# Kernel tuning notes

Hardware: AMD Instinct MI355X
Metric: run time of the kernel (lower is better)

Reference implementation:

```python
import jax, jax.numpy as jnp
import numpy as np

B, C, H, W = 2, 512, 30, 40
K = 64
PATCH, STRIDE = 4, 1
EPS = 1e-12  # torch F.normalize eps


def _l2norm(v, axis):
    n = jnp.sqrt(jnp.sum(v * v, axis=axis, keepdims=True))
    return v / jnp.maximum(n, EPS)


def setup_inputs() -> dict:
    key = jax.random.key(0)
    k1, k2, k3 = jax.random.split(key, 3)
    x = jax.random.normal(k1, (B, C, H, W), dtype=jnp.float32)
    conv_w = jax.random.normal(k2, (K, C), dtype=jnp.float32) * 0.05  # 1x1 conv weight, no bias (vlad_v2=False)
    centroids = jax.random.normal(k3, (K, C), dtype=jnp.float32)
    return {"x": x, "conv_w": conv_w, "centroids": centroids}


def reference(x, conv_w, centroids):
    b, c, h, w = x.shape
    k = centroids.shape[0]
    # input L2 normalization along channels
    xn = _l2norm(x, axis=1)
    # soft assignment: 1x1 conv + softmax over clusters
    soft = jax.nn.softmax(jnp.einsum('kc,bchw->bkhw', conv_w, xn), axis=1)
    # weighted residuals [B,K,C,H,W] (fused; original loops over K)
    resid = (xn[:, None, :, :, :] - centroids[None, :, :, None, None]) * soft[:, :, None, :, :]
    # global VLAD: sum over spatial
    vlad_global = jnp.sum(resid, axis=(-2, -1))  # [B,K,C]
    vlad_global = _l2norm(vlad_global, axis=2).reshape(b, -1)
    vlad_global = _l2norm(vlad_global, axis=1)
    # integral image over [B, K*C, H, W]
    r = resid.reshape(b, k * c, h, w)
    integ = jnp.cumsum(jnp.cumsum(r, axis=-1), axis=-2)
    integ = jnp.pad(integ, ((0, 0), (0, 0), (1, 0), (1, 0)))  # [B,KC,H+1,W+1]
    # box-sum via integral-image differences (equiv. to the dilated 2x2 grouped conv)
    p, s = PATCH, STRIDE
    hp = (h - p) // s + 1
    wp = (w - p) // s + 1
    ye, xe = (hp - 1) * s + 1, (wp - 1) * s + 1
    tl = integ[:, :, 0:ye:s, 0:xe:s]
    tr = integ[:, :, 0:ye:s, p:p + xe:s]
    bl = integ[:, :, p:p + ye:s, 0:xe:s]
    br = integ[:, :, p:p + ye:s, p:p + xe:s]
    box = (br - tr - bl + tl) / (p * p)  # [B,KC,hp,wp]
    v = box.reshape(b, k, c, hp * wp)
    v = _l2norm(v, axis=2)  # intra-cluster norm
    v = v.reshape(b, k * c, hp * wp)
    vlad_local = _l2norm(v, axis=1)  # [B, K*C, hp*wp]
    return (vlad_local, vlad_global)
```

## Files before the change

kernel.cpp:

```cpp
#include <hip/hip_runtime.h>
#include <math.h>

#define BB 2
#define CC 512
#define HH 30
#define WW 40
#define KK 64
#define NPIX (HH*WW)
#define HP 27
#define WP 37
#define NP (HP*WP)
#define LEPS 1e-12f

#define PADW 168
#define SROW 680
#define NCG 8

__global__ __launch_bounds__(512) void k_norm_soft(
    const float* __restrict__ x, const float* __restrict__ convw,
    float* __restrict__ xn, float* __restrict__ soft)
{
  const int h = blockIdx.x, b = blockIdx.y;
  const int t = threadIdx.x;
  __shared__ float xc[64][41];
  __shared__ float cw[64][65];
  __shared__ float Lb[KK][WW + 1];
  __shared__ float psum[12][WW];
  __shared__ float invn[WW];
  __shared__ float mx[WW], Zs[WW];

  const size_t xbase = (size_t)b * CC * NPIX + (size_t)h * WW;

  if (t < 480) {
    const int w = t % 40, part = t / 40;
    float s = 0.f;
    for (int c = part; c < CC; c += 12) {
      const float v = x[xbase + (size_t)c * NPIX + w];
      s = fmaf(v, v, s);
    }
    psum[part][w] = s;
  }
  __syncthreads();
  if (t < 40) {
    float s = 0.f;
    #pragma unroll
    for (int p = 0; p < 12; ++p) s += psum[p][t];
    invn[t] = 1.f / fmaxf(sqrtf(s), LEPS);
  }
  __syncthreads();

  const int k = t & 63, wp = t >> 6;
  float acc[5] = {0.f, 0.f, 0.f, 0.f, 0.f};
  for (int cb = 0; cb < CC; cb += 64) {
    #pragma unroll
    for (int n = 0; n < 5; ++n) {
      const int idx = t + 512 * n;
      const int c = idx / 40, w = idx % 40;
      const float v = x[xbase + (size_t)(cb + c) * NPIX + w] * invn[w];
      xc[c][w] = v;
      xn[xbase + (size_t)(cb + c) * NPIX + w] = v;
    }
    #pragma unroll
    for (int n = 0; n < 8; ++n) {
      const int idx = t + 512 * n;
      const int kk2 = idx >> 6, c2 = idx & 63;
      cw[kk2][c2] = convw[(size_t)kk2 * CC + cb + c2];
    }
    __syncthreads();
    #pragma unroll 1
    for (int c = 0; c < 64; ++c) {
      const float cv = cw[k][c];
      #pragma unroll
      for (int n = 0; n < 5; ++n)
        acc[n] = fmaf(cv, xc[c][wp + 8 * n], acc[n]);
    }
    __syncthreads();
  }
  #pragma unroll
  for (int n = 0; n < 5; ++n) Lb[k][wp + 8 * n] = acc[n];
  __syncthreads();
  if (t < 40) {
    float m = -1e30f;
    for (int kk2 = 0; kk2 < KK; ++kk2) m = fmaxf(m, Lb[kk2][t]);
    float Z = 0.f;
    for (int kk2 = 0; kk2 < KK; ++kk2) Z += expf(Lb[kk2][t] - m);
    mx[t] = m; Zs[t] = Z;
  }
  __syncthreads();
  const size_t sbase = (size_t)b * KK * NPIX + (size_t)h * WW;
  #pragma unroll
  for (int n = 0; n < 5; ++n) {
    const int idx = t + 512 * n;
    const int kk2 = idx / 40, w = idx % 40;
    soft[sbase + (size_t)kk2 * NPIX + w] = expf(Lb[kk2][w] - mx[w]) / Zs[w];
  }
}

__global__ __launch_bounds__(256) void k_global(
    const float* __restrict__ xn, const float* __restrict__ soft,
    const float* __restrict__ cent, float* __restrict__ ghat)
{
  const int k = blockIdx.x, b = blockIdx.y, t = threadIdx.x;
  __shared__ float sb[NPIX];
  __shared__ float red[256];
  const float* srow = soft + ((size_t)b * KK + k) * NPIX;
  for (int i2 = t; i2 < NPIX; i2 += 256) sb[i2] = srow[i2];
  __syncthreads();
  float p = 0.f;
  for (int i2 = t; i2 < NPIX; i2 += 256) p += sb[i2];
  red[t] = p;
  __syncthreads();
  for (int s = 128; s > 0; s >>= 1) { if (t < s) red[t] += red[t + s]; __syncthreads(); }
  const float Sg = red[0];
  __syncthreads();

  const int c0 = t, c1 = t + 256;
  const float* x0 = xn + ((size_t)b * CC + c0) * NPIX;
  const float* x1 = xn + ((size_t)b * CC + c1) * NPIX;
  float a0 = 0.f, a1 = 0.f;
  for (int p4 = 0; p4 < NPIX; p4 += 4) {
    const float4 s4 = *(const float4*)&sb[p4];
    const float4 v0 = *(const float4*)(x0 + p4);
    const float4 v1 = *(const float4*)(x1 + p4);
    a0 = fmaf(s4.x, v0.x, a0); a0 = fmaf(s4.y, v0.y, a0);
    a0 = fmaf(s4.z, v0.z, a0); a0 = fmaf(s4.w, v0.w, a0);
    a1 = fmaf(s4.x, v1.x, a1); a1 = fmaf(s4.y, v1.y, a1);
    a1 = fmaf(s4.z, v1.z, a1); a1 = fmaf(s4.w, v1.w, a1);
  }
  const float g0 = a0 - cent[(size_t)k * CC + c0] * Sg;
  const float g1 = a1 - cent[(size_t)k * CC + c1] * Sg;
  red[t] = g0 * g0 + g1 * g1;
  __syncthreads();
  for (int s = 128; s > 0; s >>= 1) { if (t < s) red[t] += red[t + s]; __syncthreads(); }
  const float inv = 1.f / fmaxf(sqrtf(red[0]), LEPS);
  float* gr = ghat + ((size_t)b * KK + k) * CC;
  gr[c0] = g0 * inv; gr[c1] = g1 * inv;
}

__global__ __launch_bounds__(256) void k_global2(
    const float* __restrict__ ghat, float* __restrict__ outg)
{
  const int b = blockIdx.x, t = threadIdx.x;
  __shared__ float red[256];
  const float* gb = ghat + (size_t)b * KK * CC;
  float p = 0.f;
  for (int i2 = t; i2 < KK * CC; i2 += 256) { const float v = gb[i2]; p = fmaf(v, v, p); }
  red[t] = p;
  __syncthreads();
  for (int s = 128; s > 0; s >>= 1) { if (t < s) red[t] += red[t + s]; __syncthreads(); }
  const float inv = 1.f / fmaxf(sqrtf(red[0]), LEPS);
  for (int i2 = t; i2 < KK * CC; i2 += 256)
    outg[(size_t)b * KK * CC + i2] = gb[i2] * inv;
}

template<int PHASE>
__global__ __launch_bounds__(320, 2) void k_local2(
    const float* __restrict__ xn, const float* __restrict__ soft,
    const float* __restrict__ cent, float* __restrict__ sp,
    const float* __restrict__ fs, float* __restrict__ out)
{
  const int cg = blockIdx.x;
  const int k0 = blockIdx.y * 4;
  const int bz = blockIdx.z;
  const int b = bz >> 1, iz = bz & 1;
  const int i0 = iz * 14;
  const int n_i = iz ? 13 : 14;
  const int c0 = cg * 64;
  const int t = threadIdx.x;
  const int c8 = t / 40, j = t % 40;

  __shared__ float xn_l[64][PADW];
  __shared__ float soft_l[4][SROW];
  __shared__ float cent_l[4][64];
  __shared__ float red[PHASE == 0 ? 8*4*40 : 4];

  {
    const int len = (NPIX - i0 * 40) < SROW ? (NPIX - i0 * 40) : SROW;
    const int nf4 = len >> 2;
    for (int u = t; u < 4 * nf4; u += 320) {
      const int kk = u / nf4, q = u - kk * nf4;
      *(float4*)&soft_l[kk][q * 4] =
        *(const float4*)&soft[((size_t)(b * KK + k0 + kk)) * NPIX + i0 * 40 + q * 4];
    }
  }
  if (t < 256) cent_l[t >> 6][t & 63] = cent[(size_t)(k0 + (t >> 6)) * CC + c0 + (t & 63)];

  const int sc = t / 10, sq = t % 10;
  #pragma unroll
  for (int rr = 0; rr < 4; ++rr) {
    const int row = i0 + rr;
    const int slot = (row & 3) * 40 + sq * 4;
    *(float4*)&xn_l[sc][slot] =
      *(const float4*)&xn[((size_t)(b * CC + c0 + sc)) * NPIX + (size_t)row * 40 + sq * 4];
    *(float4*)&xn_l[sc + 32][slot] =
      *(const float4*)&xn[((size_t)(b * CC + c0 + sc + 32)) * NPIX + (size_t)row * 40 + sq * 4];
  }
  __syncthreads();

  for (int ii = 0; ii < n_i; ++ii) {
    const int i = i0 + ii;

    const int nrow = (i + 4 < HH) ? (i + 4) : (HH - 1);
    const float4 st0 = *(const float4*)&xn[((size_t)(b * CC + c0 + sc)) * NPIX
                                           + (size_t)nrow * 40 + sq * 4];
    const float4 st1 = *(const float4*)&xn[((size_t)(b * CC + c0 + sc + 32)) * NPIX
                                           + (size_t)nrow * 40 + sq * 4];
    float fsv[4];
    if (PHASE == 1) {
      #pragma unroll
      for (int kk = 0; kk < 4; ++kk)
        fsv[kk] = (j < WP)
          ? fs[((size_t)(b * KK + k0 + kk)) * NP + (size_t)i * WP + j] : 0.f;
    }

    float sloc[4] = {0.f, 0.f, 0.f, 0.f};
    if (j < WP) {
      float acc[8][4];
      float Ssum[4] = {0.f, 0.f, 0.f, 0.f};
      #pragma unroll
      for (int cc = 0; cc < 8; ++cc)
        #pragma unroll
        for (int kk = 0; kk < 4; ++kk) acc[cc][kk] = 0.f;
      #pragma unroll
      for (int r = 0; r < 4; ++r) {
        const int xo = ((i + r) & 3) * 40 + j;
        const int so = (ii + r) * 40 + j;
        float sv[4][4];
        #pragma unroll
        for (int kk = 0; kk < 4; ++kk) {
          #pragma unroll
          for (int dx = 0; dx < 4; ++dx) sv[kk][dx] = soft_l[kk][so + dx];
          Ssum[kk] += (sv[kk][0] + sv[kk][1]) + (sv[kk][2] + sv[kk][3]);
        }
        #pragma unroll
        for (int cc = 0; cc < 8; ++cc) {
          const float x0 = xn_l[c8 * 8 + cc][xo + 0];
          const float x1 = xn_l[c8 * 8 + cc][xo + 1];
          const float x2 = xn_l[c8 * 8 + cc][xo + 2];
          const float x3 = xn_l[c8 * 8 + cc][xo + 3];
          #pragma unroll
          for (int kk = 0; kk < 4; ++kk) {
            float a = acc[cc][kk];
            a = fmaf(x0, sv[kk][0], a);
            a = fmaf(x1, sv[kk][1], a);
            a = fmaf(x2, sv[kk][2], a);
            a = fmaf(x3, sv[kk][3], a);
            acc[cc][kk] = a;
          }
        }
      }
      #pragma unroll
      for (int kk = 0; kk < 4; ++kk) {
        const float Sv = Ssum[kk];
        #pragma unroll
        for (int cc = 0; cc < 8; ++cc) {
          const float raw = fmaf(-cent_l[kk][c8 * 8 + cc], Sv, acc[cc][kk]);
          if (PHASE == 0)
            sloc[kk] = fmaf(raw, raw, sloc[kk]);
          else
            out[((size_t)((b * KK + k0 + kk) * CC + c0 + c8 * 8 + cc)) * NP
                + (size_t)i * WP + j] = raw * fsv[kk];
        }
      }
    }
    if (PHASE == 0) {
      #pragma unroll
      for (int kk = 0; kk < 4; ++kk) red[(c8 * 4 + kk) * 40 + j] = sloc[kk];
    }
    __syncthreads();

    {
      const int slot = ((i + 4) & 3) * 40 + sq * 4;
      *(float4*)&xn_l[sc][slot] = st0;
      *(float4*)&xn_l[sc + 32][slot] = st1;
    }
    if (PHASE == 0 && t < 160) {
      const int kk = t / 40, jj = t % 40;
      if (jj < WP) {
        float s = 0.f;
        #pragma unroll
        for (int g = 0; g < 8; ++g) s += red[(g * 4 + kk) * 40 + jj];
        sp[(((size_t)(b * KK + k0 + kk)) * NCG + cg) * NP + (size_t)i * WP + jj] = s;
      }
    }
    __syncthreads();
  }
}

__global__ __launch_bounds__(256) void k_nf_a(
    const float* __restrict__ sp, float* __restrict__ ssq)
{
  const int u = blockIdx.x * 256 + threadIdx.x;
  if (u >= BB * KK * NP) return;
  const int bk = u / NP, p = u - bk * NP;
  float s = 0.f;
  #pragma unroll
  for (int g = 0; g < NCG; ++g)
    s += sp[((size_t)bk * NCG + g) * NP + p];
  ssq[u] = s;
}

__global__ __launch_bounds__(256) void k_nf_b(
    const float* __restrict__ ssq, float* __restrict__ fs)
{
  const int b = blockIdx.y, t = threadIdx.x;
  const int k = t >> 2, dp = t & 3;
  const int p = blockIdx.x * 4 + dp;
  __shared__ float red[64][4];
  __shared__ float inv2s[4];
  const bool ok = p < NP;
  const float sr = ok ? ssq[((size_t)(b * KK + k)) * NP + p] : 0.f;
  const float iv = 1.f / fmaxf(sqrtf(sr) * 0.0625f, LEPS);
  red[k][dp] = sr * (1.f / 256.f) * iv * iv;
  __syncthreads();
  if (t < 4) {
    float s = 0.f;
    #pragma unroll
    for (int kk = 0; kk < 64; ++kk) s += red[kk][t];
    inv2s[t] = 1.f / fmaxf(sqrtf(s), LEPS);
  }
  __syncthreads();
  if (ok)
    fs[((size_t)(b * KK + k)) * NP + p] = 0.0625f * iv * inv2s[dp];
}

extern "C" void kernel_launch(void* const* d_in, const int* in_sizes, int n_in,
                              void* d_out, int out_size, void* d_ws, size_t ws_size,
                              hipStream_t stream)
{
  const float* x     = (const float*)d_in[0];
  const float* convw = (const float*)d_in[1];
  const float* cent  = (const float*)d_in[2];
  float* out = (float*)d_out;
  float* ws  = (float*)d_ws;

  float* xn   = ws;
  float* soft = xn   + (size_t)BB * CC * NPIX;
  float* fs   = soft + (size_t)BB * KK * NPIX;
  float* ghat = fs   + (size_t)BB * KK * NP;
  float* ssq  = ghat + (size_t)BB * KK * CC;
  float* sp   = ssq  + (size_t)BB * KK * NP;

  k_norm_soft<<<dim3(HH, BB), 512, 0, stream>>>(x, convw, xn, soft);
  k_global<<<dim3(KK, BB), 256, 0, stream>>>(xn, soft, cent, ghat);
  k_global2<<<dim3(BB), 256, 0, stream>>>(ghat, out + (size_t)BB * KK * CC * NP);
  k_local2<0><<<dim3(NCG, KK / 4, BB * 2), 320, 0, stream>>>(xn, soft, cent, sp, fs, out);
  k_nf_a<<<dim3((BB * KK * NP + 255) / 256), 256, 0, stream>>>(sp, ssq);
  k_nf_b<<<dim3((NP + 3) / 4, BB), 256, 0, stream>>>(ssq, fs);
  k_local2<1><<<dim3(NCG, KK / 4, BB * 2), 320, 0, stream>>>(xn, soft, cent, sp, fs, out);
}
```

Before: 382.1 us.

## Retile local VLAD kernel to 8 clusters per block with shuffle reductions

```diff
diff --git a/kernel.cpp b/kernel.cpp
--- a/kernel.cpp
+++ b/kernel.cpp
@@ -12,8 +12,7 @@
 #define NP (HP*WP)
 #define LEPS 1e-12f
 
-#define PADW 168
-#define SROW 680
+#define PADW 172
 #define NCG 8
 
 __global__ __launch_bounds__(512) void k_norm_soft(
@@ -154,36 +153,33 @@
 }
 
 template<int PHASE>
-__global__ __launch_bounds__(320, 2) void k_local2(
+__global__ __launch_bounds__(320, 4) void k_local3(
     const float* __restrict__ xn, const float* __restrict__ soft,
     const float* __restrict__ cent, float* __restrict__ sp,
     const float* __restrict__ fs, float* __restrict__ out)
 {
   const int cg = blockIdx.x;
-  const int k0 = blockIdx.y * 4;
+  const int kgrp = blockIdx.y;
   const int bz = blockIdx.z;
-  const int b = bz >> 1, iz = bz & 1;
-  const int i0 = iz * 14;
-  const int n_i = iz ? 13 : 14;
-  const int c0 = cg * 64;
+  const int b = bz >> 2, iq = bz & 3;
+  const int i0 = iq * 7;
+  const int n_i = (iq == 3) ? 6 : 7;
+  const int k0 = kgrp * 8, c0 = cg * 64;
   const int t = threadIdx.x;
-  const int c8 = t / 40, j = t % 40;
+  const int c8 = t & 7, j = t >> 3;
 
   __shared__ float xn_l[64][PADW];
-  __shared__ float soft_l[4][SROW];
-  __shared__ float cent_l[4][64];
-  __shared__ float red[PHASE == 0 ? 8*4*40 : 4];
-
-  {
-    const int len = (NPIX - i0 * 40) < SROW ? (NPIX - i0 * 40) : SROW;
-    const int nf4 = len >> 2;
-    for (int u = t; u < 4 * nf4; u += 320) {
-      const int kk = u / nf4, q = u - kk * nf4;
-      *(float4*)&soft_l[kk][q * 4] =
-        *(const float4*)&soft[((size_t)(b * KK + k0 + kk)) * NPIX + i0 * 40 + q * 4];
-    }
-  }
-  if (t < 256) cent_l[t >> 6][t & 63] = cent[(size_t)(k0 + (t >> 6)) * CC + c0 + (t & 63)];
+  __shared__ float soft_l[8][408];
+  __shared__ float cent_l[8][64];
+
+  for (int u = t; u < 8 * 400; u += 320) {
+    const int kk = u / 400, rw = u - kk * 400;
+    int row = i0 + rw / 40; if (row > HH - 1) row = HH - 1;
+    soft_l[kk][rw] = soft[((size_t)(b * KK + k0 + kk)) * NPIX
+                          + (size_t)row * 40 + (rw % 40)];
+  }
+  for (int u = t; u < 512; u += 320)
+    cent_l[u >> 6][u & 63] = cent[(size_t)(k0 + (u >> 6)) * CC + c0 + (u & 63)];
 
   const int sc = t / 10, sq = t % 10;
   #pragma unroll
@@ -205,83 +201,78 @@
                                            + (size_t)nrow * 40 + sq * 4];
     const float4 st1 = *(const float4*)&xn[((size_t)(b * CC + c0 + sc + 32)) * NPIX
                                            + (size_t)nrow * 40 + sq * 4];
-    float fsv[4];
+    float fsv[8];
     if (PHASE == 1) {
       #pragma unroll
-      for (int kk = 0; kk < 4; ++kk)
+      for (int kk = 0; kk < 8; ++kk)
         fsv[kk] = (j < WP)
           ? fs[((size_t)(b * KK + k0 + kk)) * NP + (size_t)i * WP + j] : 0.f;
     }
 
-    float sloc[4] = {0.f, 0.f, 0.f, 0.f};
-    if (j < WP) {
-      float acc[8][4];
-      float Ssum[4] = {0.f, 0.f, 0.f, 0.f};
-      #pragma unroll
-      for (int cc = 0; cc < 8; ++cc)
-        #pragma unroll
-        for (int kk = 0; kk < 4; ++kk) acc[cc][kk] = 0.f;
-      #pragma unroll
-      for (int r = 0; r < 4; ++r) {
-        const int xo = ((i + r) & 3) * 40 + j;
-        const int so = (ii + r) * 40 + j;
-        float sv[4][4];
-        #pragma unroll
-        for (int kk = 0; kk < 4; ++kk) {
+    float acc[8][8];
+    float Ssum[8];
+    #pragma unroll
+    for (int cc = 0; cc < 8; ++cc)
+      #pragma unroll
+      for (int kk = 0; kk < 8; ++kk) acc[cc][kk] = 0.f;
+    #pragma unroll
+    for (int kk = 0; kk < 8; ++kk) Ssum[kk] = 0.f;
+
+    #pragma unroll
+    for (int r = 0; r < 4; ++r) {
+      const int xo = ((i + r) & 3) * 40 + j;
+      const int so = (ii + r) * 40 + j;
+      #pragma unroll
+      for (int dx = 0; dx < 4; ++dx) {
+        float sv[8], xv[8];
+        #pragma unroll
+        for (int kk = 0; kk < 8; ++kk) {
+          sv[kk] = soft_l[kk][so + dx];
+          Ssum[kk] += sv[kk];
+        }
+        #pragma unroll
+        for (int cc = 0; cc < 8; ++cc)
+          xv[cc] = xn_l[cc * 8 + c8][xo + dx];
+        #pragma unroll
+        for (int cc = 0; cc < 8; ++cc)
           #pragma unroll
-          for (int dx = 0; dx < 4; ++dx) sv[kk][dx] = soft_l[kk][so + dx];
-          Ssum[kk] += (sv[kk][0] + sv[kk][1]) + (sv[kk][2] + sv[kk][3]);
+          for (int kk = 0; kk < 8; ++kk)
+            acc[cc][kk] = fmaf(xv[cc], sv[kk], acc[cc][kk]);
+      }
+    }
+
+    if (PHASE == 0) {
+      #pragma unroll
+      for (int kk = 0; kk < 8; ++kk) {
+        float s = 0.f;
+        #pragma unroll
+        for (int cc = 0; cc < 8; ++cc) {
+          const float raw = fmaf(-cent_l[kk][cc * 8 + c8], Ssum[kk], acc[cc][kk]);
+          s = fmaf(raw, raw, s);
         }
+        s += __shfl_xor(s, 1, 64);
+        s += __shfl_xor(s, 2, 64);
+        s += __shfl_xor(s, 4, 64);
+        if (c8 == 0 && j < WP)
+          sp[(((size_t)(b * KK + k0 + kk)) * NCG + cg) * NP + (size_t)i * WP + j] = s;
+      }
+    } else if (j < WP) {
+      #pragma unroll
+      for (int kk = 0; kk < 8; ++kk) {
         #pragma unroll
         for (int cc = 0; cc < 8; ++cc) {
-          const float x0 = xn_l[c8 * 8 + cc][xo + 0];
-          const float x1 = xn_l[c8 * 8 + cc][xo + 1];
-          const float x2 = xn_l[c8 * 8 + cc][xo + 2];
-          const float x3 = xn_l[c8 * 8 + cc][xo + 3];
-          #pragma unroll
-          for (int kk = 0; kk < 4; ++kk) {
-            float a = acc[cc][kk];
-            a = fmaf(x0, sv[kk][0], a);
-            a = fmaf(x1, sv[kk][1], a);
-            a = fmaf(x2, sv[kk][2], a);
-            a = fmaf(x3, sv[kk][3], a);
-            acc[cc][kk] = a;
-          }
+          const float raw = fmaf(-cent_l[kk][cc * 8 + c8], Ssum[kk], acc[cc][kk]);
+          out[((size_t)((b * KK + k0 + kk) * CC + c0 + cc * 8 + c8)) * NP
+              + (size_t)i * WP + j] = raw * fsv[kk];
         }
       }
-      #pragma unroll
-      for (int kk = 0; kk < 4; ++kk) {
-        const float Sv = Ssum[kk];
-        #pragma unroll
-        for (int cc = 0; cc < 8; ++cc) {
-          const float raw = fmaf(-cent_l[kk][c8 * 8 + cc], Sv, acc[cc][kk]);
-          if (PHASE == 0)
-            sloc[kk] = fmaf(raw, raw, sloc[kk]);
-          else
-            out[((size_t)((b * KK + k0 + kk) * CC + c0 + c8 * 8 + cc)) * NP
-                + (size_t)i * WP + j] = raw * fsv[kk];
-        }
-      }
-    }
-    if (PHASE == 0) {
-      #pragma unroll
-      for (int kk = 0; kk < 4; ++kk) red[(c8 * 4 + kk) * 40 + j] = sloc[kk];
-    }
+    }
+
     __syncthreads();
-
     {
       const int slot = ((i + 4) & 3) * 40 + sq * 4;
       *(float4*)&xn_l[sc][slot] = st0;
       *(float4*)&xn_l[sc + 32][slot] = st1;
-    }
-    if (PHASE == 0 && t < 160) {
-      const int kk = t / 40, jj = t % 40;
-      if (jj < WP) {
-        float s = 0.f;
-        #pragma unroll
-        for (int g = 0; g < 8; ++g) s += red[(g * 4 + kk) * 40 + jj];
-        sp[(((size_t)(b * KK + k0 + kk)) * NCG + cg) * NP + (size_t)i * WP + jj] = s;
-      }
     }
     __syncthreads();
   }
@@ -344,8 +335,8 @@
   k_norm_soft<<<dim3(HH, BB), 512, 0, stream>>>(x, convw, xn, soft);
   k_global<<<dim3(KK, BB), 256, 0, stream>>>(xn, soft, cent, ghat);
   k_global2<<<dim3(BB), 256, 0, stream>>>(ghat, out + (size_t)BB * KK * CC * NP);
-  k_local2<0><<<dim3(NCG, KK / 4, BB * 2), 320, 0, stream>>>(xn, soft, cent, sp, fs, out);
+  k_local3<0><<<dim3(NCG, KK / 8, BB * 4), 320, 0, stream>>>(xn, soft, cent, sp, fs, out);
   k_nf_a<<<dim3((BB * KK * NP + 255) / 256), 256, 0, stream>>>(sp, ssq);
   k_nf_b<<<dim3((NP + 3) / 4, BB), 256, 0, stream>>>(ssq, fs);
-  k_local2<1><<<dim3(NCG, KK / 4, BB * 2), 320, 0, stream>>>(xn, soft, cent, sp, fs, out);
-}
+  k_local3<1><<<dim3(NCG, KK / 8, BB * 4), 320, 0, stream>>>(xn, soft, cent, sp, fs, out);
+}
```

Result: slower. 526.8 us (+37.9%).

## Replace two-pass local VLAD recompute with raw write plus in-place scaling pass

Applied to the files above, without the earlier changes.

```diff
diff --git a/kernel.cpp b/kernel.cpp
--- a/kernel.cpp
+++ b/kernel.cpp
@@ -137,8 +137,8 @@
   gr[c0] = g0 * inv; gr[c1] = g1 * inv;
 }
 
-__global__ __launch_bounds__(256) void k_global2(
-    const float* __restrict__ ghat, float* __restrict__ outg)
+__global__ __launch_bounds__(256) void k_g2a(
+    const float* __restrict__ ghat, float* __restrict__ inv2g)
 {
   const int b = blockIdx.x, t = threadIdx.x;
   __shared__ float red[256];
@@ -148,16 +148,23 @@
   red[t] = p;
   __syncthreads();
   for (int s = 128; s > 0; s >>= 1) { if (t < s) red[t] += red[t + s]; __syncthreads(); }
-  const float inv = 1.f / fmaxf(sqrtf(red[0]), LEPS);
-  for (int i2 = t; i2 < KK * CC; i2 += 256)
-    outg[(size_t)b * KK * CC + i2] = gb[i2] * inv;
-}
-
-template<int PHASE>
-__global__ __launch_bounds__(320, 2) void k_local2(
+  if (t == 0) inv2g[b] = 1.f / fmaxf(sqrtf(red[0]), LEPS);
+}
+
+__global__ __launch_bounds__(256) void k_g2b(
+    const float* __restrict__ ghat, const float* __restrict__ inv2g,
+    float* __restrict__ outg)
+{
+  const int b = blockIdx.y;
+  const int u = blockIdx.x * 256 + threadIdx.x;
+  if (u < KK * CC)
+    outg[(size_t)b * KK * CC + u] = ghat[(size_t)b * KK * CC + u] * inv2g[b];
+}
+
+__global__ __launch_bounds__(320, 2) void k_rawssq(
     const float* __restrict__ xn, const float* __restrict__ soft,
     const float* __restrict__ cent, float* __restrict__ sp,
-    const float* __restrict__ fs, float* __restrict__ out)
+    float* __restrict__ out)
 {
   const int cg = blockIdx.x;
   const int k0 = blockIdx.y * 4;
@@ -172,7 +179,7 @@
   __shared__ float xn_l[64][PADW];
   __shared__ float soft_l[4][SROW];
   __shared__ float cent_l[4][64];
-  __shared__ float red[PHASE == 0 ? 8*4*40 : 4];
+  __shared__ float red[8 * 4 * 40];
 
   {
     const int len = (NPIX - i0 * 40) < SROW ? (NPIX - i0 * 40) : SROW;
@@ -205,13 +212,6 @@
                                            + (size_t)nrow * 40 + sq * 4];
     const float4 st1 = *(const float4*)&xn[((size_t)(b * CC + c0 + sc + 32)) * NPIX
                                            + (size_t)nrow * 40 + sq * 4];
-    float fsv[4];
-    if (PHASE == 1) {
-      #pragma unroll
-      for (int kk = 0; kk < 4; ++kk)
-        fsv[kk] = (j < WP)
-          ? fs[((size_t)(b * KK + k0 + kk)) * NP + (size_t)i * WP + j] : 0.f;
-    }
 
     float sloc[4] = {0.f, 0.f, 0.f, 0.f};
     if (j < WP) {
@@ -255,18 +255,14 @@
         #pragma unroll
         for (int cc = 0; cc < 8; ++cc) {
           const float raw = fmaf(-cent_l[kk][c8 * 8 + cc], Sv, acc[cc][kk]);
-          if (PHASE == 0)
-            sloc[kk] = fmaf(raw, raw, sloc[kk]);
-          else
-            out[((size_t)((b * KK + k0 + kk) * CC + c0 + c8 * 8 + cc)) * NP
-                + (size_t)i * WP + j] = raw * fsv[kk];
+          sloc[kk] = fmaf(raw, raw, sloc[kk]);
+          out[((size_t)((b * KK + k0 + kk) * CC + c0 + c8 * 8 + cc)) * NP
+              + (size_t)i * WP + j] = raw;
         }
       }
     }
-    if (PHASE == 0) {
-      #pragma unroll
-      for (int kk = 0; kk < 4; ++kk) red[(c8 * 4 + kk) * 40 + j] = sloc[kk];
-    }
+    #pragma unroll
+    for (int kk = 0; kk < 4; ++kk) red[(c8 * 4 + kk) * 40 + j] = sloc[kk];
     __syncthreads();
 
     {
@@ -274,7 +270,7 @@
       *(float4*)&xn_l[sc][slot] = st0;
       *(float4*)&xn_l[sc + 32][slot] = st1;
     }
-    if (PHASE == 0 && t < 160) {
+    if (t < 160) {
       const int kk = t / 40, jj = t % 40;
       if (jj < WP) {
         float s = 0.f;
@@ -287,21 +283,8 @@
   }
 }
 
-__global__ __launch_bounds__(256) void k_nf_a(
-    const float* __restrict__ sp, float* __restrict__ ssq)
-{
-  const int u = blockIdx.x * 256 + threadIdx.x;
-  if (u >= BB * KK * NP) return;
-  const int bk = u / NP, p = u - bk * NP;
-  float s = 0.f;
-  #pragma unroll
-  for (int g = 0; g < NCG; ++g)
-    s += sp[((size_t)bk * NCG + g) * NP + p];
-  ssq[u] = s;
-}
-
-__global__ __launch_bounds__(256) void k_nf_b(
-    const float* __restrict__ ssq, float* __restrict__ fs)
+__global__ __launch_bounds__(256) void k_nf(
+    const float* __restrict__ sp, float* __restrict__ fs)
 {
   const int b = blockIdx.y, t = threadIdx.x;
   const int k = t >> 2, dp = t & 3;
@@ -309,7 +292,12 @@
   __shared__ float red[64][4];
   __shared__ float inv2s[4];
   const bool ok = p < NP;
-  const float sr = ok ? ssq[((size_t)(b * KK + k)) * NP + p] : 0.f;
+  float sr = 0.f;
+  if (ok) {
+    #pragma unroll
+    for (int g = 0; g < NCG; ++g)
+      sr += sp[(((size_t)(b * KK + k)) * NCG + g) * NP + p];
+  }
   const float iv = 1.f / fmaxf(sqrtf(sr) * 0.0625f, LEPS);
   red[k][dp] = sr * (1.f / 256.f) * iv * iv;
   __syncthreads();
@@ -322,6 +310,27 @@
   __syncthreads();
   if (ok)
     fs[((size_t)(b * KK + k)) * NP + p] = 0.0625f * iv * inv2s[dp];
+}
+
+__global__ __launch_bounds__(256) void k_scale(
+    float* __restrict__ outr, const float* __restrict__ fs)
+{
+  const size_t NV = (size_t)BB * KK * CC * NP / 4;
+  const int CPN = CC * NP;
+  for (size_t v = (size_t)blockIdx.x * 256 + threadIdx.x; v < NV;
+       v += (size_t)gridDim.x * 256) {
+    const size_t base = v * 4;
+    const int bk = (int)(base / CPN);
+    const int rem = (int)(base - (size_t)bk * CPN);
+    int p0 = rem % NP;
+    const float* fb = fs + (size_t)bk * NP;
+    const int p1 = (p0 + 1 == NP) ? 0 : p0 + 1;
+    const int p2 = (p1 + 1 == NP) ? 0 : p1 + 1;
+    const int p3 = (p2 + 1 == NP) ? 0 : p2 + 1;
+    float4 o = *(float4*)&outr[base];
+    o.x *= fb[p0]; o.y *= fb[p1]; o.z *= fb[p2]; o.w *= fb[p3];
+    *(float4*)&outr[base] = o;
+  }
 }
 
 extern "C" void kernel_launch(void* const* d_in, const int* in_sizes, int n_in,
@@ -334,18 +343,20 @@
   float* out = (float*)d_out;
   float* ws  = (float*)d_ws;
 
-  float* xn   = ws;
-  float* soft = xn   + (size_t)BB * CC * NPIX;
-  float* fs   = soft + (size_t)BB * KK * NPIX;
-  float* ghat = fs   + (size_t)BB * KK * NP;
-  float* ssq  = ghat + (size_t)BB * KK * CC;
-  float* sp   = ssq  + (size_t)BB * KK * NP;
+  float* xn    = ws;
+  float* soft  = xn    + (size_t)BB * CC * NPIX;
+  float* fs    = soft  + (size_t)BB * KK * NPIX;
+  float* ghat  = fs    + (size_t)BB * KK * NP;
+  float* sp    = ghat  + (size_t)BB * KK * CC;
+  float* inv2g = sp    + (size_t)BB * KK * NCG * NP;
+
+  float* outg = out + (size_t)BB * KK * CC * NP;
 
   k_norm_soft<<<dim3(HH, BB), 512, 0, stream>>>(x, convw, xn, soft);
+  k_rawssq<<<dim3(NCG, KK / 4, BB * 2), 320, 0, stream>>>(xn, soft, cent, sp, out);
   k_global<<<dim3(KK, BB), 256, 0, stream>>>(xn, soft, cent, ghat);
-  k_global2<<<dim3(BB), 256, 0, stream>>>(ghat, out + (size_t)BB * KK * CC * NP);
-  k_local2<0><<<dim3(NCG, KK / 4, BB * 2), 320, 0, stream>>>(xn, soft, cent, sp, fs, out);
-  k_nf_a<<<dim3((BB * KK * NP + 255) / 256), 256, 0, stream>>>(sp, ssq);
-  k_nf_b<<<dim3((NP + 3) / 4, BB), 256, 0, stream>>>(ssq, fs);
-  k_local2<1><<<dim3(NCG, KK / 4, BB * 2), 320, 0, stream>>>(xn, soft, cent, sp, fs, out);
-}
+  k_g2a<<<dim3(BB), 256, 0, stream>>>(ghat, inv2g);
+  k_g2b<<<dim3((KK * CC + 255) / 256, BB), 256, 0, stream>>>(ghat, inv2g, outg);
+  k_nf<<<dim3((NP + 3) / 4, BB), 256, 0, stream>>>(sp, fs);
+  k_scale<<<dim3(2048), 256, 0, stream>>>(out, fs);
+}
```

After: 415.8 us. +8.8%, slower.
